# Performance work log

Measured on AMD Instinct MI355X. Metric: run time of the kernel, lower is better.

Reference implementation:

```python
import jax, jax.numpy as jnp
import numpy as np
from jax import lax

V = 5001   # vocab_size = len(word2id)+1
E = 128    # embedding_dim
H = 256    # hidden_dim
HH = H // 2  # per-direction hidden
T = 9      # tag_len
B, S = 256, 512


def setup_inputs() -> dict:
    key = jax.random.key(0)
    ks = jax.random.split(key, 16)
    sc = 0.08
    n = lambda k, shp: (jax.random.normal(k, shp) * sc).astype(jnp.float32)
    return {
        "x": jax.random.randint(ks[0], (B, S), 0, V),
        "mask": jnp.ones((B, S), jnp.float32),
        "embed_table": n(ks[1], (V, E)),
        "Wih_f": n(ks[2], (4 * HH, E)), "Whh_f": n(ks[3], (4 * HH, HH)),
        "bih_f": n(ks[4], (4 * HH,)), "bhh_f": n(ks[5], (4 * HH,)),
        "Wih_b": n(ks[6], (4 * HH, E)), "Whh_b": n(ks[7], (4 * HH, HH)),
        "bih_b": n(ks[8], (4 * HH,)), "bhh_b": n(ks[9], (4 * HH,)),
        "W_out": n(ks[10], (T, H)), "b_out": n(ks[11], (T,)),
        "transitions": n(ks[12], (T, T)),
        "start_trans": n(ks[13], (T,)),
        "end_trans": n(ks[14], (T,)),
    }


def _lstm_dir(xs, Wih, Whh, bih, bhh, reverse):
    # xs: [S,B,E]; torch gate order i,f,g,o
    Bx = xs.shape[1]
    h0 = jnp.zeros((Bx, HH), xs.dtype)
    pre_x = jnp.einsum('sbe,ge->sbg', xs, Wih) + bih + bhh  # hoist input proj

    def step(carry, px):
        h, c = carry
        g = px + h @ Whh.T
        i, f, gg, o = jnp.split(g, 4, axis=-1)
        c = jax.nn.sigmoid(f) * c + jax.nn.sigmoid(i) * jnp.tanh(gg)
        h = jax.nn.sigmoid(o) * jnp.tanh(c)
        return (h, c), h

    _, hs = lax.scan(step, (h0, h0), pre_x, reverse=reverse)
    return hs  # [S,B,HH]


def _viterbi(emissions, mask, transitions, start_trans, end_trans):
    # emissions: [B,S,T], mask: [B,S] bool -> tags [B,S] int32, best score [B]
    Bx = emissions.shape[0]
    em_t = emissions.transpose(1, 0, 2)        # [S,B,T]
    score0 = start_trans + em_t[0]             # [B,T]
    idT = jnp.arange(T, dtype=jnp.int32)

    def step(score, inp):
        em, m = inp                            # em [B,T], m [B]
        cand = score[:, :, None] + transitions[None]     # [B,Tprev,Tcur]
        best = jnp.max(cand, axis=1) + em
        bp = jnp.argmax(cand, axis=1).astype(jnp.int32)  # [B,T]
        new_score = jnp.where(m[:, None], best, score)
        bp = jnp.where(m[:, None], bp, idT[None, :])
        return new_score, bp

    score, bps = lax.scan(step, score0, (em_t[1:], mask.T[1:]))  # bps [S-1,B,T]
    score = score + end_trans
    best_score = jnp.max(score, axis=-1)                          # [B]
    last = jnp.argmax(score, axis=-1).astype(jnp.int32)           # [B]

    def back(tag, bp_t):
        prev = jnp.take_along_axis(bp_t, tag[:, None], axis=1)[:, 0]
        return prev, prev

    _, prevs = lax.scan(back, last, bps, reverse=True)            # [S-1,B]
    tags = jnp.concatenate([prevs, last[None, :]], axis=0).T      # [B,S]
    return tags, best_score


def reference(x, mask, embed_table, Wih_f, Whh_f, bih_f, bhh_f,
              Wih_b, Whh_b, bih_b, bhh_b, W_out, b_out,
              transitions, start_trans, end_trans):
    emb = embed_table[x]                       # [B,S,E]
    xs = emb.transpose(1, 0, 2)                # [S,B,E]
    hf = _lstm_dir(xs, Wih_f, Whh_f, bih_f, bhh_f, reverse=False)
    hb = _lstm_dir(xs, Wih_b, Whh_b, bih_b, bhh_b, reverse=True)
    hs = jnp.concatenate([hf, hb], axis=-1).transpose(1, 0, 2)   # [B,S,H]
    # dropout is identity at inference
    em = hs @ W_out.T + b_out                  # [B,S,T]
    em = em * mask[..., None]
    tags, best_score = _viterbi(em, mask > 0, transitions, start_trans, end_trans)
    return tags, best_score
```

## Files before the change

### kernel.cpp

```cpp
#include <hip/hip_runtime.h>
#include <hip/hip_bf16.h>
#include <math.h>

#define S_LEN 512
#define B_SZ  256
#define E_DIM 128
#define HHID  128
#define G4    512
#define T_TAG 9
#define VOCAB 5001
#define VOCABP 5008
#define EMP_SZ (512L * 16 * 256)

typedef __attribute__((ext_vector_type(8))) short bf16x8;
typedef __attribute__((ext_vector_type(4))) float f32x4;
typedef __attribute__((ext_vector_type(8))) unsigned short u16x8;

__device__ __forceinline__ float bf2f(__hip_bfloat16 v) { return __bfloat162float(v); }
__device__ __forceinline__ float scrub0(float v) {
    unsigned u = __float_as_uint(v);
    return (((u >> 23) & 0xFFu) == 0xFFu) ? 0.f : v;
}
__device__ __forceinline__ float frcp(float x) { return __builtin_amdgcn_rcpf(x); }
__device__ __forceinline__ float fsig(float x) { return frcp(1.f + __expf(-x)); }
__device__ __forceinline__ float ftanh(float x) {
    return 1.f - 2.f * frcp(1.f + __expf(2.f * x));
}

__device__ __hip_bfloat16 g_emb[VOCAB * E_DIM];
__device__ __hip_bfloat16 g_wih[2][G4 * E_DIM];
__device__ __hip_bfloat16 g_whh2[2][G4 * HHID];
__device__ __align__(16) float g_bias[2][G4];
__device__ float g_wout[T_TAG * 256];
__device__ float g_bout[T_TAG];
__device__ float g_trans[T_TAG * T_TAG];
__device__ float g_start[T_TAG];
__device__ float g_end[T_TAG];
__device__ float g_maskf[B_SZ * S_LEN];
__device__ __align__(16) float g_pxv[(long)2 * VOCABP * 128 * 4];
__device__ __align__(16) float g_emp[8][EMP_SZ];

__global__ __launch_bounds__(256) void convert_kernel(
    const void* mask, const void* emb,
    const void* wih_f, const void* whh_f, const void* bih_f, const void* bhh_f,
    const void* wih_b, const void* whh_b, const void* bih_b, const void* bhh_b,
    const void* wout, const void* bout, const void* trans,
    const void* startt, const void* endt, float* out, int out_size)
{
    const bool isb = (((const unsigned*)mask)[0] == 0x3F803F80u);
    auto ldf = [&](const void* p, long i) -> float {
        float v = isb ? bf2f(((const __hip_bfloat16*)p)[i]) : ((const float*)p)[i];
        return scrub0(v);
    };
    const long tid0   = (long)blockIdx.x * blockDim.x + threadIdx.x;
    const long stride = (long)gridDim.x * blockDim.x;

    for (long i = tid0; i < out_size; i += stride) out[i] = 0.f;

    if (isb) {
        const u16x8* src = (const u16x8*)emb;
        u16x8* dst = (u16x8*)g_emb;
        for (long i = tid0; i < (long)VOCAB * E_DIM / 8; i += stride) {
            u16x8 v = src[i];
            #pragma unroll
            for (int j = 0; j < 8; j++)
                if (((v[j] >> 7) & 0xFFu) == 0xFFu) v[j] = 0;
            dst[i] = v;
        }
    } else {
        const float4* src = (const float4*)emb;
        for (long i = tid0; i < (long)VOCAB * E_DIM / 4; i += stride) {
            const float4 v = src[i];
            __hip_bfloat16* d = &g_emb[i * 4];
            d[0] = __float2bfloat16(scrub0(v.x));
            d[1] = __float2bfloat16(scrub0(v.y));
            d[2] = __float2bfloat16(scrub0(v.z));
            d[3] = __float2bfloat16(scrub0(v.w));
        }
    }
    for (long i = tid0; i < (long)G4 * E_DIM; i += stride) {
        const int np = (int)(i >> 7), e = (int)(i & 127);
        const int g = np & 3, u = np >> 2;
        const long src = (long)(g * 128 + u) * E_DIM + e;
        g_wih[0][i] = __float2bfloat16(ldf(wih_f, src));
        g_wih[1][i] = __float2bfloat16(ldf(wih_b, src));
    }
    for (long i = tid0; i < (long)G4 * HHID; i += stride) {
        const int np = (int)(i >> 7), k = (int)(i & 127);
        const int g = np & 3, u = np >> 2;
        const long src = (long)(g * 128 + u) * HHID + k;
        g_whh2[0][i] = __float2bfloat16(ldf(whh_f, src));
        g_whh2[1][i] = __float2bfloat16(ldf(whh_b, src));
    }
    for (long i = tid0; i < G4; i += stride) {
        const int g = (int)i & 3, u = (int)i >> 2;
        const long src = g * 128 + u;
        g_bias[0][i] = ldf(bih_f, src) + ldf(bhh_f, src);
        g_bias[1][i] = ldf(bih_b, src) + ldf(bhh_b, src);
    }
    for (long i = tid0; i < T_TAG * 256; i += stride) g_wout[i] = ldf(wout, i);
    for (long i = tid0; i < T_TAG * T_TAG; i += stride) g_trans[i] = ldf(trans, i);
    for (long i = tid0; i < T_TAG; i += stride) {
        g_bout[i]  = ldf(bout, i);
        g_start[i] = ldf(startt, i);
        g_end[i]   = ldf(endt, i);
    }
    for (long i = tid0; i < (long)B_SZ * S_LEN; i += stride)
        g_maskf[i] = ldf(mask, i);
}

__global__ __launch_bounds__(512, 2) void pxv_gemm()
{
    const int grp = blockIdx.x, dir = blockIdx.y;
    const int tid  = threadIdx.x;
    const int lane = tid & 63, wv = tid >> 6;
    const int m16  = lane & 15, quad = lane >> 4;

    bf16x8 V[4][4];
    f32x4 bias4[4];
    #pragma unroll
    for (int t = 0; t < 4; t++) {
        const int np = (wv * 4 + t) * 16 + m16;
        #pragma unroll
        for (int kk = 0; kk < 4; kk++)
            V[t][kk] = *(const bf16x8*)&g_wih[dir][(long)np * E_DIM + kk * 32 + quad * 8];
        const int u = 16 * wv + 4 * t + quad;
        const float4 b4 = *(const float4*)&g_bias[dir][4 * u];
        bias4[t] = (f32x4){b4.x, b4.y, b4.z, b4.w};
    }
    const int v  = grp * 16 + m16;
    const int vv = (v < VOCAB) ? v : 0;
    bf16x8 E[4];
    #pragma unroll
    for (int kk = 0; kk < 4; kk++)
        E[kk] = *(const bf16x8*)&g_emb[(long)vv * E_DIM + kk * 32 + quad * 8];
    #pragma unroll
    for (int t = 0; t < 4; t++) {
        f32x4 px = bias4[t];
        #pragma unroll
        for (int kk = 0; kk < 4; kk++)
            px = __builtin_amdgcn_mfma_f32_16x16x32_bf16(V[t][kk], E[kk], px, 0, 0, 0);
        const int u = 16 * wv + 4 * t + quad;
        if (v < VOCAB)
            *(f32x4*)&g_pxv[((long)(dir * VOCABP + v) * 128 + u) * 4] = px;
    }
}

#define SCAN_STEP(RD, PX)                                                      \
  {                                                                            \
    const int wr_ = (RD) ^ 1;                                                  \
        \
    int se2_ = sev + 2 * step;                                                 \
    se2_ = se2_ < 0 ? 0 : (se2_ > S_LEN - 1 ? S_LEN - 1 : se2_);               \
    const float* pf_ = pxvL + xO[se2_ * 16 + m16];                             \
    bf16x8 Hh_[4], Hl_[4];                                                     \
    _Pragma("unroll")                                                          \
    for (int kk = 0; kk < 4; kk++) {                                           \
        const int off_ = ((kk * 4 + quad) * 16 + m16) * 8;                     \
        Hh_[kk] = *(const bf16x8*)&hB[RD][0][off_];                            \
        Hl_[kk] = *(const bf16x8*)&hB[RD][1][off_];                            \
    }                                                                          \
    _Pragma("unroll")                                                          \
    for (int t = 0; t < 4; t++) {                                              \
        _Pragma("unroll")                                                      \
        for (int kk = 0; kk < 4; kk++) {                                       \
            PX[t] = __builtin_amdgcn_mfma_f32_16x16x32_bf16(W[t][kk], Hh_[kk], PX[t], 0, 0, 0); \
            PX[t] = __builtin_amdgcn_mfma_f32_16x16x32_bf16(W[t][kk], Hl_[kk], PX[t], 0, 0, 0); \
        }                                                                      \
    }                                                                          \
         \
    if (wv < 4 && itv) {                                                       \
        f32x4 em_ = {0.f, 0.f, 0.f, 0.f};                                      \
        _Pragma("unroll")                                                      \
        for (int kk = 0; kk < 4; kk++)                                         \
            em_ = __builtin_amdgcn_mfma_f32_16x16x32_bf16(                     \
                WA[kk], (wv & 1) ? Hl_[kk] : Hh_[kk], em_, 0, 0, 0);           \
        empq[0]  = em_[0];                                                     \
        empq[16] = em_[1];                                                     \
        empq[32] = em_[2];                                                     \
        empq[48] = em_[3];                                                     \
    }                                                                          \
    _Pragma("unroll")                                                          \
    for (int t = 0; t < 4; t++) {                                              \
        const float iv = fsig(PX[t][0]);                                       \
        const float fv = fsig(PX[t][1]);                                       \
        const float gv = ftanh(PX[t][2]);                                      \
        const float ov = fsig(PX[t][3]);                                       \
        c[t] = fv * c[t] + iv * gv;                                            \
        const float h = ov * ftanh(c[t]);                                      \
        const int u = 16 * wv + 4 * t + quad;                                  \
        const unsigned ub = __float_as_uint(h);                                \
        const unsigned hb_ = ub >> 16;                                         \
        const float hif = __uint_as_float(ub & 0xFFFF0000u);                   \
        const unsigned lb_ = __float_as_uint(h - hif) >> 16;                   \
        const int ha = (u >> 3) * 128 + m16 * 8 + (u & 7);                     \
        hB[wr_][0][ha] = (unsigned short)hb_;                                  \
        hB[wr_][1][ha] = (unsigned short)lb_;                                  \
    }                                                                          \
    {          \
        PX[0] = *(const f32x4*)(pf_ + 0);                                      \
        PX[1] = *(const f32x4*)(pf_ + 16);                                     \
        PX[2] = *(const f32x4*)(pf_ + 32);                                     \
        PX[3] = *(const f32x4*)(pf_ + 48);                                     \
    }                                                                          \
    asm volatile("s_waitcnt lgkmcnt(0)" ::: "memory");                         \
    __builtin_amdgcn_sched_barrier(0);                                         \
    __builtin_amdgcn_s_barrier();                                              \
    __builtin_amdgcn_sched_barrier(0);                                         \
    empq = empp; empp += empd; sev += step; itv++;                             \
  }

__global__ __launch_bounds__(512, 2) void scan_mfma(const int* __restrict__ x)
{
    __shared__ __align__(16) unsigned short hB[2][2][16 * 16 * 8];
    __shared__ int xO[S_LEN * 16];

    const int bg = blockIdx.x, dir = blockIdx.y;
    const int tid  = threadIdx.x;
    const int lane = tid & 63, wv = tid >> 6;
    const int m16  = lane & 15, quad = lane >> 4;

    bf16x8 W[4][4];
    #pragma unroll
    for (int t = 0; t < 4; t++) {
        const int np = (wv * 4 + t) * 16 + m16;
        #pragma unroll
        for (int kk = 0; kk < 4; kk++)
            W[t][kk] = *(const bf16x8*)&g_whh2[dir][(long)np * HHID + kk * 32 + quad * 8];
    }
    bf16x8 WA[4];
    if (wv < 4) {
        #pragma unroll
        for (int kk = 0; kk < 4; kk++) {
            #pragma unroll
            for (int j = 0; j < 8; j++) {
                const float w = (m16 < T_TAG)
                    ? g_wout[m16 * 256 + dir * 128 + kk * 32 + quad * 8 + j] : 0.f;
                const unsigned uw  = __float_as_uint(w);
                const unsigned hib = uw >> 16;
                const float hif    = __uint_as_float(uw & 0xFFFF0000u);
                const unsigned lob = __float_as_uint(w - hif) >> 16;
                WA[kk][j] = (short)((wv < 2) ? hib : lob);
            }
        }
    }
    {
        const bool x64 = ((x[1] | x[3] | x[5] | x[7]) == 0);
        for (int i = tid; i < S_LEN * 16; i += 512) {
            const int s = i >> 4, m = i & 15;
            const int ii = (bg * 16 + m) * S_LEN + s;
            int tok = x64 ? x[2 * ii] : x[ii];
            tok = (unsigned)tok < VOCAB ? tok : 0;
            xO[i] = tok * 512;
        }
    }
    for (int i = tid; i < 2 * 2 * 2048; i += 512) ((unsigned short*)hB)[i] = 0;
    float c[4] = {0.f, 0.f, 0.f, 0.f};
    __syncthreads();

    const int se0  = dir ? (S_LEN - 1) : 0;
    const int step = dir ? -1 : 1;
    const int u0   = 16 * wv + quad;

    const float* pxvL = &g_pxv[(long)dir * VOCABP * 512 + u0 * 4];

    f32x4 pxA[4], pxB[4];
    {
        const int o0 = xO[se0 * 16 + m16];
        #pragma unroll
        for (int t = 0; t < 4; t++) pxA[t] = *(const f32x4*)(pxvL + o0 + 16 * t);
        const int se1 = (S_LEN > 1) ? se0 + step : se0;
        const int o1 = xO[se1 * 16 + m16];
        #pragma unroll
        for (int t = 0; t < 4; t++) pxB[t] = *(const f32x4*)(pxvL + o1 + 16 * t);
    }

    float* empp = &g_emp[dir * 4 + (wv & 3)]
                        [((long)(se0 * 16 + bg)) * 256 + (quad * 4) * 16 + m16];
    const long empd = (long)step * 4096;
    float* empq = empp;

    int itv = 0, sev = se0;

    for (int it = 0; it < S_LEN; it += 2) {
        SCAN_STEP(0, pxA)
        SCAN_STEP(1, pxB)
    }

    if (wv < 4) {
        bf16x8 Hh_[4], Hl_[4];
        #pragma unroll
        for (int kk = 0; kk < 4; kk++) {
            const int off_ = ((kk * 4 + quad) * 16 + m16) * 8;
            Hh_[kk] = *(const bf16x8*)&hB[0][0][off_];
            Hl_[kk] = *(const bf16x8*)&hB[0][1][off_];
        }
        f32x4 em_ = {0.f, 0.f, 0.f, 0.f};
        #pragma unroll
        for (int kk = 0; kk < 4; kk++)
            em_ = __builtin_amdgcn_mfma_f32_16x16x32_bf16(
                WA[kk], (wv & 1) ? Hl_[kk] : Hh_[kk], em_, 0, 0, 0);
        empq[0]  = em_[0];
        empq[16] = em_[1];
        empq[32] = em_[2];
        empq[48] = em_[3];
    }
}

__global__ __launch_bounds__(64, 1)
void viterbi_kernel(float* __restrict__ out, int out_size)
{
    __shared__ unsigned char bp[S_LEN][T_TAG];
    const int lane = threadIdx.x;
    const int b  = blockIdx.x;
    const int jj = (lane < T_TAG) ? lane : 0;
    const int bg = b >> 4, mm = b & 15;

    float tcol[T_TAG];
    #pragma unroll
    for (int i = 0; i < T_TAG; i++) tcol[i] = g_trans[i * T_TAG + jj];
    const float boj = g_bout[jj];

    float score[T_TAG];
    {
        const float m0 = g_maskf[b * S_LEN + 0];
        #pragma unroll
        for (int i = 0; i < T_TAG; i++) {
            const long o = (long)bg * 256 + i * 16 + mm;
            const float s8 = (((g_emp[0][o] + g_emp[1][o]) + (g_emp[2][o] + g_emp[3][o]))
                            + ((g_emp[4][o] + g_emp[5][o]) + (g_emp[6][o] + g_emp[7][o])));
            score[i] = g_start[i] + scrub0(g_bout[i] + s8) * m0;
        }
    }
    long off = 4096L + (long)bg * 256 + jj * 16 + mm;
    float p0 = g_emp[0][off], p1 = g_emp[1][off], p2 = g_emp[2][off], p3 = g_emp[3][off];
    float p4 = g_emp[4][off], p5 = g_emp[5][off], p6 = g_emp[6][off], p7 = g_emp[7][off];
    float m = g_maskf[b * S_LEN + 1];

    for (int s = 1; s < S_LEN; s++) {
        const long offn = off + 4096;
        float q0 = 0.f, q1 = 0.f, q2 = 0.f, q3 = 0.f;
        float q4 = 0.f, q5 = 0.f, q6 = 0.f, q7 = 0.f, mn = 0.f;
        if (s + 1 < S_LEN) {
            q0 = g_emp[0][offn]; q1 = g_emp[1][offn];
            q2 = g_emp[2][offn]; q3 = g_emp[3][offn];
            q4 = g_emp[4][offn]; q5 = g_emp[5][offn];
            q6 = g_emp[6][offn]; q7 = g_emp[7][offn];
            mn = g_maskf[b * S_LEN + s + 1];
        }
        const float e = scrub0(boj + (((p0 + p1) + (p2 + p3)) + ((p4 + p5) + (p6 + p7))));
        float best = score[0] + tcol[0];
        int arg = 0;
        #pragma unroll
        for (int i = 1; i < T_TAG; i++) {
            const float cnd = score[i] + tcol[i];
            if (cnd > best) { best = cnd; arg = i; }
        }
        float ns; int nbp;
        if (m > 0.f) { ns = best + e * m; nbp = arg; }
        else         { ns = score[jj];    nbp = jj;  }
        if (lane < T_TAG) bp[s][jj] = (unsigned char)nbp;
        #pragma unroll
        for (int i = 0; i < T_TAG; i++) score[i] = __shfl(ns, i, 64);
        p0 = q0; p1 = q1; p2 = q2; p3 = q3;
        p4 = q4; p5 = q5; p6 = q6; p7 = q7;
        m = mn; off = offn;
    }
    #pragma unroll
    for (int i = 0; i < T_TAG; i++) score[i] += g_end[i];

    __syncthreads();

    if (lane == 0) {
        float bs = score[0]; int last = 0;
        #pragma unroll
        for (int i = 1; i < T_TAG; i++)
            if (score[i] > bs) { bs = score[i]; last = i; }
        {
            const unsigned u = __float_as_uint(bs);
            if (((u >> 23) & 0xFFu) == 0xFFu) bs = -100.f;
        }
        if ((long)B_SZ * S_LEN + b < out_size)
            out[(long)B_SZ * S_LEN + b] = bs;
        int tag = last;
        if (tag < 0) tag = 0; if (tag > 8) tag = 8;
        out[(long)b * S_LEN + (S_LEN - 1)] = (float)tag;
        for (int s2 = S_LEN - 1; s2 >= 1; s2--) {
            tag = bp[s2][tag];
            if (tag < 0) tag = 0; if (tag > 8) tag = 8;
            out[(long)b * S_LEN + (s2 - 1)] = (float)tag;
        }
    }
}

extern "C" void kernel_launch(void* const* d_in, const int* in_sizes, int n_in,
                              void* d_out, int out_size, void* d_ws, size_t ws_size,
                              hipStream_t stream) {
    const int* x = (const int*)d_in[0];
    float* out = (float*)d_out;

    convert_kernel<<<512, 256, 0, stream>>>(
        d_in[1], d_in[2], d_in[3], d_in[4], d_in[5], d_in[6],
        d_in[7], d_in[8], d_in[9], d_in[10], d_in[11], d_in[12],
        d_in[13], d_in[14], d_in[15], out, out_size);
    pxv_gemm<<<dim3((VOCABP / 16), 2), 512, 0, stream>>>();
    scan_mfma<<<dim3(16, 2), 512, 0, stream>>>(x);
    viterbi_kernel<<<256, 64, 0, stream>>>(out, out_size);
}
```

Measured before the change: 931.5 us.

## Interleave emission partials for vector loads and deepen Viterbi prefetch

Changes the emission-partial buffer from eight separate planes to two planes, with the four wave partials interleaved so each Viterbi step reads two 16-byte vectors instead of eight scalars. The Viterbi loop is unrolled by two and prefetches two steps ahead to hide global-load latency on its serial critical path. The LSTM writer now stores with a stride of 4, scattering its stores more, which may cost some store efficiency in the scan kernel.

```diff
diff --git a/kernel.cpp b/kernel.cpp
--- a/kernel.cpp
+++ b/kernel.cpp
@@ -38,7 +38,7 @@
 __device__ float g_end[T_TAG];
 __device__ float g_maskf[B_SZ * S_LEN];
 __device__ __align__(16) float g_pxv[(long)2 * VOCABP * 128 * 4];
-__device__ __align__(16) float g_emp[8][EMP_SZ];
+__device__ __align__(16) float g_emp[2][EMP_SZ * 4];
 
 __global__ __launch_bounds__(256) void convert_kernel(
     const void* mask, const void* emb,
@@ -175,10 +175,10 @@
         for (int kk = 0; kk < 4; kk++)                                         \
             em_ = __builtin_amdgcn_mfma_f32_16x16x32_bf16(                     \
                 WA[kk], (wv & 1) ? Hl_[kk] : Hh_[kk], em_, 0, 0, 0);           \
-        empq[0]  = em_[0];                                                     \
-        empq[16] = em_[1];                                                     \
-        empq[32] = em_[2];                                                     \
-        empq[48] = em_[3];                                                     \
+        empq[0]   = em_[0];                                                    \
+        empq[64]  = em_[1];                                                    \
+        empq[128] = em_[2];                                                    \
+        empq[192] = em_[3];                                                    \
     }                                                                          \
     _Pragma("unroll")                                                          \
     for (int t = 0; t < 4; t++) {                                              \
@@ -275,9 +275,9 @@
         for (int t = 0; t < 4; t++) pxB[t] = *(const f32x4*)(pxvL + o1 + 16 * t);
     }
 
-    float* empp = &g_emp[dir * 4 + (wv & 3)]
-                        [((long)(se0 * 16 + bg)) * 256 + (quad * 4) * 16 + m16];
-    const long empd = (long)step * 4096;
+    float* empp = &g_emp[dir]
+        [(((long)(se0 * 16 + bg) * 256 + quad * 64 + m16) << 2) + (wv & 3)];
+    const long empd = (long)step * 16384;
     float* empq = empp;
 
     int itv = 0, sev = se0;
@@ -300,12 +300,39 @@
         for (int kk = 0; kk < 4; kk++)
             em_ = __builtin_amdgcn_mfma_f32_16x16x32_bf16(
                 WA[kk], (wv & 1) ? Hl_[kk] : Hh_[kk], em_, 0, 0, 0);
-        empq[0]  = em_[0];
-        empq[16] = em_[1];
-        empq[32] = em_[2];
-        empq[48] = em_[3];
-    }
-}
+        empq[0]   = em_[0];
+        empq[64]  = em_[1];
+        empq[128] = em_[2];
+        empq[192] = em_[3];
+    }
+}
+
+#define VLOAD(S, A, C, M)                                                      \
+  {                                                                            \
+    const long e_ = ((long)((S) * 16 + bg) * 256 + jj * 16 + mm) << 2;         \
+    A = *(const f32x4*)&g_emp[0][e_];                                          \
+    C = *(const f32x4*)&g_emp[1][e_];                                          \
+    M = g_maskf[b * S_LEN + (S)];                                              \
+  }
+
+#define VSTEP(S, A, C, M)                                                      \
+  {                                                                            \
+    const float e = scrub0(boj + (((A[0] + A[1]) + (A[2] + A[3]))              \
+                                + ((C[0] + C[1]) + (C[2] + C[3]))));           \
+    float best = score[0] + tcol[0];                                           \
+    int arg = 0;                                                               \
+    _Pragma("unroll")                                                          \
+    for (int i = 1; i < T_TAG; i++) {                                          \
+        const float cnd = score[i] + tcol[i];                                  \
+        if (cnd > best) { best = cnd; arg = i; }                               \
+    }                                                                          \
+    float ns; int nbp;                                                         \
+    if (M > 0.f) { ns = best + e * M; nbp = arg; }                             \
+    else         { ns = score[jj];    nbp = jj;  }                             \
+    if (lane < T_TAG) bp[S][jj] = (unsigned char)nbp;                          \
+    _Pragma("unroll")                                                          \
+    for (int i = 0; i < T_TAG; i++) score[i] = __shfl(ns, i, 64);              \
+  }
 
 __global__ __launch_bounds__(64, 1)
 void viterbi_kernel(float* __restrict__ out, int out_size)
@@ -326,45 +353,29 @@
         const float m0 = g_maskf[b * S_LEN + 0];
         #pragma unroll
         for (int i = 0; i < T_TAG; i++) {
-            const long o = (long)bg * 256 + i * 16 + mm;
-            const float s8 = (((g_emp[0][o] + g_emp[1][o]) + (g_emp[2][o] + g_emp[3][o]))
-                            + ((g_emp[4][o] + g_emp[5][o]) + (g_emp[6][o] + g_emp[7][o])));
+            const long o = ((long)bg * 256 + i * 16 + mm) << 2;
+            const f32x4 A = *(const f32x4*)&g_emp[0][o];
+            const f32x4 C = *(const f32x4*)&g_emp[1][o];
+            const float s8 = (((A[0] + A[1]) + (A[2] + A[3]))
+                            + ((C[0] + C[1]) + (C[2] + C[3])));
             score[i] = g_start[i] + scrub0(g_bout[i] + s8) * m0;
         }
     }
-    long off = 4096L + (long)bg * 256 + jj * 16 + mm;
-    float p0 = g_emp[0][off], p1 = g_emp[1][off], p2 = g_emp[2][off], p3 = g_emp[3][off];
-    float p4 = g_emp[4][off], p5 = g_emp[5][off], p6 = g_emp[6][off], p7 = g_emp[7][off];
-    float m = g_maskf[b * S_LEN + 1];
-
-    for (int s = 1; s < S_LEN; s++) {
-        const long offn = off + 4096;
-        float q0 = 0.f, q1 = 0.f, q2 = 0.f, q3 = 0.f;
-        float q4 = 0.f, q5 = 0.f, q6 = 0.f, q7 = 0.f, mn = 0.f;
-        if (s + 1 < S_LEN) {
-            q0 = g_emp[0][offn]; q1 = g_emp[1][offn];
-            q2 = g_emp[2][offn]; q3 = g_emp[3][offn];
-            q4 = g_emp[4][offn]; q5 = g_emp[5][offn];
-            q6 = g_emp[6][offn]; q7 = g_emp[7][offn];
-            mn = g_maskf[b * S_LEN + s + 1];
-        }
-        const float e = scrub0(boj + (((p0 + p1) + (p2 + p3)) + ((p4 + p5) + (p6 + p7))));
-        float best = score[0] + tcol[0];
-        int arg = 0;
-        #pragma unroll
-        for (int i = 1; i < T_TAG; i++) {
-            const float cnd = score[i] + tcol[i];
-            if (cnd > best) { best = cnd; arg = i; }
-        }
-        float ns; int nbp;
-        if (m > 0.f) { ns = best + e * m; nbp = arg; }
-        else         { ns = score[jj];    nbp = jj;  }
-        if (lane < T_TAG) bp[s][jj] = (unsigned char)nbp;
-        #pragma unroll
-        for (int i = 0; i < T_TAG; i++) score[i] = __shfl(ns, i, 64);
-        p0 = q0; p1 = q1; p2 = q2; p3 = q3;
-        p4 = q4; p5 = q5; p6 = q6; p7 = q7;
-        m = mn; off = offn;
+
+    f32x4 a0, c0, a1, c1, a2, c2, a3, c3;
+    float m0_, m1_, m2_, m3_;
+    VLOAD(1, a0, c0, m0_)
+    VLOAD(2, a1, c1, m1_)
+
+    for (int s = 1; s < S_LEN; s += 2) {
+        const int s2 = (s + 2 < S_LEN) ? s + 2 : s;
+        VLOAD(s2, a2, c2, m2_)
+        VSTEP(s, a0, c0, m0_)
+        const int s3 = (s + 3 < S_LEN) ? s + 3 : s;
+        VLOAD(s3, a3, c3, m3_)
+        if (s + 1 < S_LEN) VSTEP(s + 1, a1, c1, m1_)
+        a0 = a2; c0 = c2; m0_ = m2_;
+        a1 = a3; c1 = c3; m1_ = m3_;
     }
     #pragma unroll
     for (int i = 0; i < T_TAG; i++) score[i] += g_end[i];
```

Result: no change. 922.2 us (-1.0%).
